# Kernel tuning notes

Measured on AMD Instinct MI355X. Metric: run time of the kernel, lower is better.

Reference implementation:

```python
import jax, jax.numpy as jnp
import numpy as np

B, M, K, N = 4, 2048, 4096, 4096


def setup_inputs() -> dict:
    key = jax.random.key(0)
    k1, k2, k3, k4, k5 = jax.random.split(key, 5)
    # int8 quantized activations and weights (stored as int8, like the torch buffers)
    x_q = jax.random.randint(k1, (B, M, K), -128, 127, dtype=jnp.int8)
    weight = jax.random.randint(k2, (N, K), -128, 127, dtype=jnp.int8)
    # per-token activation scales and per-output-row weight scales (symmetric quant)
    scales_x = jax.random.uniform(k3, (B, M, 1), dtype=jnp.float32) * 0.01 + 1e-4
    weight_scales = jax.random.uniform(k4, (N, 1), dtype=jnp.float32) * 0.01 + 1e-4
    bias = jax.random.normal(k5, (N,), dtype=jnp.float32)
    return {"x_q": x_q, "scales_x": scales_x, "weight": weight,
            "weight_scales": weight_scales, "bias": bias}


def reference(x_q, scales_x, weight, weight_scales, bias):
    # int8 GEMM accumulating in int32: (B*M, K) @ (K, N) with weight stored (N, K)
    acc = jnp.einsum(
        'bmk,nk->bmn',
        x_q.astype(jnp.int32), weight.astype(jnp.int32),
        preferred_element_type=jnp.int32,
    )  # [B, M, N] int32
    # symmetric dequant: row (token) scale * column (output-channel) scale, then bias
    out = acc.astype(jnp.float32) * scales_x * weight_scales[:, 0] + bias
    return out.astype(jnp.float16)
```

## Files before the change

### kernel.cpp

```cpp
#include <hip/hip_runtime.h>

typedef int v4i __attribute__((ext_vector_type(4)));

constexpr int Kdim = 4096;
constexpr int Ndim = 4096;
constexpr int MtotC = 8192;
constexpr int BM = 256;
constexpr int BN = 256;
constexpr int BKB = 128;
constexpr int NT = Kdim / BKB;

#define AS1 __attribute__((address_space(1)))
#define AS3 __attribute__((address_space(3)))

__global__ void pack_i32_to_i8(const int* __restrict__ xq, const int* __restrict__ wq,
                               signed char* __restrict__ x8, signed char* __restrict__ w8,
                               size_t nx4, size_t nw4) {
    size_t i = (size_t)blockIdx.x * blockDim.x + threadIdx.x;
    size_t stride = (size_t)gridDim.x * blockDim.x;
    size_t tot = nx4 + nw4;
    for (size_t j = i; j < tot; j += stride) {
        if (j < nx4) {
            const int4 v = ((const int4*)xq)[j];
            char4 c;
            c.x = (signed char)v.x; c.y = (signed char)v.y;
            c.z = (signed char)v.z; c.w = (signed char)v.w;
            ((char4*)x8)[j] = c;
        } else {
            const size_t k = j - nx4;
            const int4 v = ((const int4*)wq)[k];
            char4 c;
            c.x = (signed char)v.x; c.y = (signed char)v.y;
            c.z = (signed char)v.z; c.w = (signed char)v.w;
            ((char4*)w8)[k] = c;
        }
    }
}

__global__ __launch_bounds__(512, 2) void i8gemm_kernel(
    const signed char* __restrict__ A,
    const signed char* __restrict__ W,
    const float* __restrict__ sx,
    const float* __restrict__ wsc,
    const float* __restrict__ bias,
    float* __restrict__ C)
{
    extern __shared__ signed char smem[];

    const int tid  = threadIdx.x;
    const int wave = tid >> 6;
    const int lane = tid & 63;
    const int wr = wave >> 2;
    const int wc = wave & 3;

    const int xr_ = blockIdx.x & 7;
    const int idx = blockIdx.x >> 3;
    const int bm = ((xr_ & 3) * 8 + (idx & 7)) * BM;
    const int bn = ((xr_ >> 2) * 8 + (idx >> 3)) * BN;

    const int srow  = tid >> 2;
    const int gslot = (tid & 3) ^ ((srow >> 1) & 3);
    const signed char* Ag = A + (size_t)(bm + srow) * Kdim + gslot * 16;
    const signed char* Wg = W + (size_t)(bn + srow) * Kdim + gslot * 16;
    const int sdst = srow * 64 + (tid & 3) * 16;

    const int frow = lane & 15;
    const int fsl  = lane >> 4;
    const int rsw  = ((fsl ^ ((frow >> 1) & 3)) << 4);
    const int aro  = (wr * 128 + frow) * 64 + rsw;
    const int bro  = 16384 + (wc * 64 + frow) * 64 + rsw;

    v4i acc[8][4];
#pragma unroll
    for (int f = 0; f < 8; ++f)
#pragma unroll
        for (int g = 0; g < 4; ++g)
#pragma unroll
            for (int e = 0; e < 4; ++e) acc[f][g][e] = 0;

    v4i avA[8], bvA[4], avB[8], bvB[4];

#define STG_HALF(KT, HALF) do {                                                        \
    signed char* dst = smem + ((KT) & 1) * 65536 + (HALF) * 32768 + sdst;              \
    const signed char* sa = Ag + (size_t)(KT) * BKB + (HALF) * 64;                     \
    const signed char* sb = Wg + (size_t)(KT) * BKB + (HALF) * 64;                     \
    __builtin_amdgcn_global_load_lds((const AS1 void*)sa,                  (AS3 void*)dst,           16, 0, 0); \
    __builtin_amdgcn_global_load_lds((const AS1 void*)(sa + (size_t)128 * Kdim), (AS3 void*)(dst + 8192),  16, 0, 0); \
    __builtin_amdgcn_global_load_lds((const AS1 void*)sb,                  (AS3 void*)(dst + 16384), 16, 0, 0); \
    __builtin_amdgcn_global_load_lds((const AS1 void*)(sb + (size_t)128 * Kdim), (AS3 void*)(dst + 24576), 16, 0, 0); \
} while (0)

#define READ_SET(AV, BV, BASE, HALF) do {                                              \
    _Pragma("unroll") for (int g_ = 0; g_ < 4; ++g_)                                   \
        BV[g_] = *(const v4i*)((BASE) + (HALF) * 32768 + bro + g_ * 1024);             \
    _Pragma("unroll") for (int f_ = 0; f_ < 8; ++f_)                                   \
        AV[f_] = *(const v4i*)((BASE) + (HALF) * 32768 + aro + f_ * 1024);             \
} while (0)

#define MFMA_SET(AV, BV) do {                                                          \
    __builtin_amdgcn_s_setprio(1);                                                     \
    _Pragma("unroll") for (int f_ = 0; f_ < 8; ++f_)                                   \
    _Pragma("unroll") for (int g_ = 0; g_ < 4; ++g_)                                   \
        acc[f_][g_] = __builtin_amdgcn_mfma_i32_16x16x64_i8(AV[f_], BV[g_], acc[f_][g_], 0, 0, 0); \
    __builtin_amdgcn_s_setprio(0);                                                     \
} while (0)

#define BAR   __builtin_amdgcn_s_barrier()
#define LGKM0 asm volatile("s_waitcnt lgkmcnt(0)" ::: "memory")

    STG_HALF(0, 0);
    STG_HALF(0, 1);
    STG_HALF(1, 0);
    STG_HALF(1, 1);
    asm volatile("s_waitcnt vmcnt(12)" ::: "memory");
    BAR;
    READ_SET(avA, bvA, smem, 0);

    for (int u = 0; u < NT - 2; ++u) {
        signed char* bufc = smem + (u & 1) * 65536;
        signed char* bufn = smem + ((u + 1) & 1) * 65536;
        asm volatile("s_waitcnt vmcnt(8)" ::: "memory");
        BAR;
        STG_HALF(u + 2, 0);
        READ_SET(avB, bvB, bufc, 1);
        MFMA_SET(avA, bvA);
        LGKM0;
        asm volatile("s_waitcnt vmcnt(8)" ::: "memory");
        BAR;
        STG_HALF(u + 2, 1);
        READ_SET(avA, bvA, bufn, 0);
        MFMA_SET(avB, bvB);
        LGKM0;
    }

    {
        signed char* bufc = smem;
        signed char* bufn = smem + 65536;
        asm volatile("s_waitcnt vmcnt(8)" ::: "memory");
        BAR;
        READ_SET(avB, bvB, bufc, 1);
        MFMA_SET(avA, bvA);
        LGKM0;
        asm volatile("s_waitcnt vmcnt(4)" ::: "memory");
        BAR;
        READ_SET(avA, bvA, bufn, 0);
        MFMA_SET(avB, bvB);
        LGKM0;
    }
    {
        signed char* bufc = smem + 65536;
        asm volatile("s_waitcnt vmcnt(0)" ::: "memory");
        BAR;
        READ_SET(avB, bvB, bufc, 1);
        MFMA_SET(avA, bvA);
        LGKM0;
        MFMA_SET(avB, bvB);
    }

    const int orow0 = bm + wr * 128;
    const int ocol0 = bn + wc * 64;
    float wsv[4], bvv[4];
#pragma unroll
    for (int g = 0; g < 4; ++g) {
        const int col = ocol0 + g * 16 + frow;
        wsv[g] = wsc[col];
        bvv[g] = bias[col];
    }
#pragma unroll
    for (int f = 0; f < 8; ++f) {
#pragma unroll
        for (int jr = 0; jr < 4; ++jr) {
            const int row = orow0 + f * 16 + fsl * 4 + jr;
            const float s = sx[row];
#pragma unroll
            for (int g = 0; g < 4; ++g) {
                const int col = ocol0 + g * 16 + frow;
                C[(size_t)row * Ndim + col] = (float)acc[f][g][jr] * s * wsv[g] + bvv[g];
            }
        }
    }
#undef STG_HALF
#undef READ_SET
#undef MFMA_SET
#undef BAR
#undef LGKM0
}

extern "C" void kernel_launch(void* const* d_in, const int* in_sizes, int n_in,
                              void* d_out, int out_size, void* d_ws, size_t ws_size,
                              hipStream_t stream) {
    (void)in_sizes; (void)n_in; (void)out_size; (void)ws_size;
    const int*   x_q  = (const int*)d_in[0];
    const float* sx   = (const float*)d_in[1];
    const int*   w_q  = (const int*)d_in[2];
    const float* wsc  = (const float*)d_in[3];
    const float* bias = (const float*)d_in[4];
    float* out = (float*)d_out;

    signed char* x8 = (signed char*)d_ws;
    signed char* w8 = x8 + (size_t)MtotC * Kdim;

    const size_t nx = (size_t)MtotC * Kdim;
    const size_t nw = (size_t)Ndim * Kdim;

    pack_i32_to_i8<<<3072, 256, 0, stream>>>(x_q, w_q, x8, w8, nx / 4, nw / 4);

    static bool attr_set = false;
    if (!attr_set) {
        hipFuncSetAttribute((const void*)i8gemm_kernel,
                            hipFuncAttributeMaxDynamicSharedMemorySize, 131072);
        attr_set = true;
    }

    const int nwg = (MtotC / BM) * (Ndim / BN);
    i8gemm_kernel<<<nwg, 512, 131072, stream>>>(x8, w8, sx, wsc, bias, out);
}
```

Baseline: 187.9 us.

## Switch to four-slot half-tile ring with deeper prefetch and partial LDS waits

Restructures the main loop so shared memory is treated as a ring of four 64-wide K half-tiles rather than two double-buffered 128-wide tiles. Global-to-LDS loads are issued three half-tiles ahead instead of two. The loop now waits with lgkmcnt(12) and a sched_barrier, so MFMAs start once the register fragments they consume are ready instead of draining all LDS reads. This aims to hide more global latency and overlap LDS reads with MFMA, at the cost of tighter waitcnt correctness and hand-counted pipeline prologue and epilogue.

```diff
diff --git a/kernel.cpp b/kernel.cpp
--- a/kernel.cpp
+++ b/kernel.cpp
@@ -7,8 +7,7 @@
 constexpr int MtotC = 8192;
 constexpr int BM = 256;
 constexpr int BN = 256;
-constexpr int BKB = 128;
-constexpr int NT = Kdim / BKB;
+constexpr int NH = 64;
 
 #define AS1 __attribute__((address_space(1)))
 #define AS3 __attribute__((address_space(3)))
@@ -80,21 +79,24 @@
 
     v4i avA[8], bvA[4], avB[8], bvB[4];
 
-#define STG_HALF(KT, HALF) do {                                                        \
-    signed char* dst = smem + ((KT) & 1) * 65536 + (HALF) * 32768 + sdst;              \
-    const signed char* sa = Ag + (size_t)(KT) * BKB + (HALF) * 64;                     \
-    const signed char* sb = Wg + (size_t)(KT) * BKB + (HALF) * 64;                     \
-    __builtin_amdgcn_global_load_lds((const AS1 void*)sa,                  (AS3 void*)dst,           16, 0, 0); \
+#define REG_OF(M) ((((M) >> 1) & 1) * 65536 + ((M) & 1) * 32768)
+
+#define STG_HALF(M) do {                                                               \
+    signed char* dst = smem + REG_OF(M) + sdst;                                        \
+    const signed char* sa = Ag + (size_t)(M) * 64;                                     \
+    const signed char* sb = Wg + (size_t)(M) * 64;                                     \
+    __builtin_amdgcn_global_load_lds((const AS1 void*)sa,                        (AS3 void*)dst,           16, 0, 0); \
     __builtin_amdgcn_global_load_lds((const AS1 void*)(sa + (size_t)128 * Kdim), (AS3 void*)(dst + 8192),  16, 0, 0); \
-    __builtin_amdgcn_global_load_lds((const AS1 void*)sb,                  (AS3 void*)(dst + 16384), 16, 0, 0); \
+    __builtin_amdgcn_global_load_lds((const AS1 void*)sb,                        (AS3 void*)(dst + 16384), 16, 0, 0); \
     __builtin_amdgcn_global_load_lds((const AS1 void*)(sb + (size_t)128 * Kdim), (AS3 void*)(dst + 24576), 16, 0, 0); \
 } while (0)
 
-#define READ_SET(AV, BV, BASE, HALF) do {                                              \
+#define READ_SET(AV, BV, M) do {                                                       \
+    const signed char* base_ = smem + REG_OF(M);                                       \
     _Pragma("unroll") for (int g_ = 0; g_ < 4; ++g_)                                   \
-        BV[g_] = *(const v4i*)((BASE) + (HALF) * 32768 + bro + g_ * 1024);             \
+        BV[g_] = *(const v4i*)(base_ + bro + g_ * 1024);                               \
     _Pragma("unroll") for (int f_ = 0; f_ < 8; ++f_)                                   \
-        AV[f_] = *(const v4i*)((BASE) + (HALF) * 32768 + aro + f_ * 1024);             \
+        AV[f_] = *(const v4i*)(base_ + aro + f_ * 1024);                               \
 } while (0)
 
 #define MFMA_SET(AV, BV) do {                                                          \
@@ -105,57 +107,55 @@
     __builtin_amdgcn_s_setprio(0);                                                     \
 } while (0)
 
-#define BAR   __builtin_amdgcn_s_barrier()
-#define LGKM0 asm volatile("s_waitcnt lgkmcnt(0)" ::: "memory")
-
-    STG_HALF(0, 0);
-    STG_HALF(0, 1);
-    STG_HALF(1, 0);
-    STG_HALF(1, 1);
-    asm volatile("s_waitcnt vmcnt(12)" ::: "memory");
-    BAR;
-    READ_SET(avA, bvA, smem, 0);
-
-    for (int u = 0; u < NT - 2; ++u) {
-        signed char* bufc = smem + (u & 1) * 65536;
-        signed char* bufn = smem + ((u + 1) & 1) * 65536;
-        asm volatile("s_waitcnt vmcnt(8)" ::: "memory");
+#define BAR     __builtin_amdgcn_s_barrier()
+#define LGKM12  do { asm volatile("s_waitcnt lgkmcnt(12)" ::: "memory");               \
+                     __builtin_amdgcn_sched_barrier(0); } while (0)
+#define LGKM0   do { asm volatile("s_waitcnt lgkmcnt(0)" ::: "memory");                \
+                     __builtin_amdgcn_sched_barrier(0); } while (0)
+#define VMC(N)  asm volatile("s_waitcnt vmcnt(" #N ")" ::: "memory")
+
+    STG_HALF(0);
+    STG_HALF(1);
+    STG_HALF(2);
+    VMC(8);
+    BAR;
+    READ_SET(avA, bvA, 0);
+
+    for (int u = 0; u < 30; ++u) {
+        const int q = 2 * u;
+        VMC(4);
         BAR;
-        STG_HALF(u + 2, 0);
-        READ_SET(avB, bvB, bufc, 1);
+        STG_HALF(q + 3);
+        READ_SET(avB, bvB, q + 1);
+        LGKM12;
         MFMA_SET(avA, bvA);
-        LGKM0;
-        asm volatile("s_waitcnt vmcnt(8)" ::: "memory");
+        VMC(4);
         BAR;
-        STG_HALF(u + 2, 1);
-        READ_SET(avA, bvA, bufn, 0);
+        STG_HALF(q + 4);
+        READ_SET(avA, bvA, q + 2);
+        LGKM12;
         MFMA_SET(avB, bvB);
-        LGKM0;
-    }
-
-    {
-        signed char* bufc = smem;
-        signed char* bufn = smem + 65536;
-        asm volatile("s_waitcnt vmcnt(8)" ::: "memory");
-        BAR;
-        READ_SET(avB, bvB, bufc, 1);
-        MFMA_SET(avA, bvA);
-        LGKM0;
-        asm volatile("s_waitcnt vmcnt(4)" ::: "memory");
-        BAR;
-        READ_SET(avA, bvA, bufn, 0);
-        MFMA_SET(avB, bvB);
-        LGKM0;
-    }
-    {
-        signed char* bufc = smem + 65536;
-        asm volatile("s_waitcnt vmcnt(0)" ::: "memory");
-        BAR;
-        READ_SET(avB, bvB, bufc, 1);
-        MFMA_SET(avA, bvA);
-        LGKM0;
-        MFMA_SET(avB, bvB);
-    }
+    }
+
+    VMC(4);
+    BAR;
+    STG_HALF(63);
+    READ_SET(avB, bvB, 61);
+    LGKM12;
+    MFMA_SET(avA, bvA);
+    VMC(4);
+    BAR;
+    READ_SET(avA, bvA, 62);
+    LGKM12;
+    MFMA_SET(avB, bvB);
+
+    VMC(0);
+    BAR;
+    READ_SET(avB, bvB, 63);
+    LGKM12;
+    MFMA_SET(avA, bvA);
+    LGKM0;
+    MFMA_SET(avB, bvB);
 
     const int orow0 = bm + wr * 128;
     const int ocol0 = bn + wc * 64;
@@ -179,11 +179,14 @@
             }
         }
     }
+#undef REG_OF
 #undef STG_HALF
 #undef READ_SET
 #undef MFMA_SET
 #undef BAR
+#undef LGKM12
 #undef LGKM0
+#undef VMC
 }
 
 extern "C" void kernel_launch(void* const* d_in, const int* in_sizes, int n_in,
```

Result: no change. 188.1 us (+0.1%).
